# Optimization experiments

Measured on AMD Instinct MI355X. Metric: run time of the kernel, lower is better.

The kernel has to match this reference:

```python
import jax, jax.numpy as jnp
import numpy as np

B, NVEC, DIM, HEADS, DH, M, ITERS, DEPTH, NCLASS, KER = 8, 4096, 512, 8, 64, 256, 6, 2, 10, 33
INNER = HEADS * DH


def _ln(x, g, b, eps=1e-5):
    mu = x.mean(-1, keepdims=True)
    var = ((x - mu) ** 2).mean(-1, keepdims=True)
    return (x - mu) * jax.lax.rsqrt(var + eps) * g + b


def _mp_pinv(x, iters=ITERS):
    # Moore-Penrose pseudo-inverse via Newton-Schulz iterations (lucidrains).
    # x: [b, h, m, m]
    abs_x = jnp.abs(x)
    col = abs_x.sum(-1).max(-1)  # [b, h]
    row = abs_x.sum(-2).max(-1)  # [b, h]
    z = jnp.swapaxes(x, -1, -2) / (col * row)[..., None, None]
    I = jnp.eye(x.shape[-1], dtype=x.dtype)
    for _ in range(iters):
        xz = x @ z
        z = 0.25 * z @ (13.0 * I - xz @ (15.0 * I - xz @ (7.0 * I - xz)))
    return z


def _nystrom_attn(x, qkv_w, out_w, out_b, conv_w):
    b, n, _ = x.shape
    qkv = x @ qkv_w  # [b, n, 3*inner]
    q, k, v = jnp.split(qkv, 3, axis=-1)
    to_h = lambda t: t.reshape(b, n, HEADS, DH).transpose(0, 2, 1, 3)  # [b,h,n,dh]
    q, k, v = to_h(q), to_h(k), to_h(v)
    q = q * (DH ** -0.5)

    l = n // M  # tokens per landmark segment (n divisible by M)
    q_l = q.reshape(b, HEADS, M, l, DH).mean(3)  # [b,h,M,dh]
    k_l = k.reshape(b, HEADS, M, l, DH).mean(3)

    attn1 = jax.nn.softmax(jnp.einsum('bhnd,bhmd->bhnm', q, k_l), axis=-1)    # [b,h,n,M]
    attn2 = jax.nn.softmax(jnp.einsum('bhmd,bhld->bhml', q_l, k_l), axis=-1)  # [b,h,M,M]
    attn3 = jax.nn.softmax(jnp.einsum('bhmd,bhnd->bhmn', q_l, k), axis=-1)    # [b,h,M,n]

    out = (attn1 @ _mp_pinv(attn2)) @ (attn3 @ v)  # [b,h,n,dh]

    # residual depthwise conv over sequence dim (kernel 33, groups=heads, no bias)
    out = out + jax.lax.conv_general_dilated(
        v, conv_w, (1, 1), [(KER // 2, KER // 2), (0, 0)],
        dimension_numbers=('NCHW', 'OIHW', 'NCHW'), feature_group_count=HEADS)

    out = out.transpose(0, 2, 1, 3).reshape(b, n, INNER)
    return out @ out_w + out_b


def setup_inputs():
    key = jax.random.key(0)
    ks = jax.random.split(key, 12)
    s = 0.02
    f32 = jnp.float32
    return {
        'x': jax.random.normal(ks[0], (B, NVEC, 2), f32),
        'lin_w': jax.random.normal(ks[1], (2, DIM), f32) * s,
        'lin_b': jnp.zeros((DIM,), f32),
        'ln1_g': jnp.ones((DEPTH, DIM), f32),
        'ln1_b': jnp.zeros((DEPTH, DIM), f32),
        'qkv_w': jax.random.normal(ks[2], (DEPTH, DIM, 3 * INNER), f32) * s,
        'out_w': jax.random.normal(ks[3], (DEPTH, INNER, DIM), f32) * s,
        'out_b': jnp.zeros((DEPTH, DIM), f32),
        'conv_w': jax.random.normal(ks[4], (DEPTH, HEADS, 1, KER, 1), f32) * s,
        'ln2_g': jnp.ones((DEPTH, DIM), f32),
        'ln2_b': jnp.zeros((DEPTH, DIM), f32),
        'ff1_w': jax.random.normal(ks[5], (DEPTH, DIM, 4 * DIM), f32) * s,
        'ff1_b': jnp.zeros((DEPTH, 4 * DIM), f32),
        'ff2_w': jax.random.normal(ks[6], (DEPTH, 4 * DIM, DIM), f32) * s,
        'ff2_b': jnp.zeros((DEPTH, DIM), f32),
        'final_w': jax.random.normal(ks[7], (NVEC * DIM, NCLASS), f32) * s,
        'final_b': jnp.zeros((NCLASS,), f32),
    }


def reference(x, lin_w, lin_b, ln1_g, ln1_b, qkv_w, out_w, out_b, conv_w,
              ln2_g, ln2_b, ff1_w, ff1_b, ff2_w, ff2_b, final_w, final_b):
    h = x @ lin_w + lin_b  # [B, NVEC, DIM]
    for i in range(DEPTH):
        h = h + _nystrom_attn(_ln(h, ln1_g[i], ln1_b[i]), qkv_w[i], out_w[i], out_b[i], conv_w[i])
        z = _ln(h, ln2_g[i], ln2_b[i])
        h = h + (jax.nn.gelu(z @ ff1_w[i] + ff1_b[i]) @ ff2_w[i] + ff2_b[i])
    return h.reshape(h.shape[0], -1) @ final_w + final_b  # [B, NCLASS]
```

## Files before the change

kernel.cpp:

```cpp
#include <hip/hip_runtime.h>
#include <hip/hip_bf16.h>

#define BB_ 8
#define NVEC 4096
#define DIM 512
#define HEADS 8
#define DH 64
#define MM_ 256
#define ITERS 6
#define DEPTH 2
#define NCLASS 10
#define KER 33
#define INNER 512
#define LSEG 16

typedef long long ll;
typedef __bf16 bh16;
typedef __attribute__((ext_vector_type(8))) __bf16 bf16x8;
typedef __attribute__((ext_vector_type(4))) float f32x4;

template<int WR, int WC, bool TRB, bool GELU_ACT, bool RESID, bool BF16OUT,
         bool DUAL, bool SMAX, bool ADDC>
__global__ void __launch_bounds__(256)
mgemm_k(const bh16* __restrict__ A, const bh16* __restrict__ B,
        const float* __restrict__ bias, void* __restrict__ Cv, void* __restrict__ C2v,
        int K, int lda, int ldb, int ldc,
        int BI, ll sAo, ll sAi, ll sBo, ll sBi, ll sCo, ll sCi,
        int ldc2, ll sC2o, ll sC2i,
        float alpha, float diagv)
{
    constexpr int BM = WR * 64, BN = WC * 64;
    const int bz = blockIdx.z;
    const int bo = bz / BI, bi = bz % BI;
    const bh16* Ab = A + bo * sAo + (ll)bi * sAi;
    const bh16* Bb = B + bo * sBo + (ll)bi * sBi;
    const ll coff = bo * sCo + (ll)bi * sCi;

    const int gx = gridDim.x;
    const int nwg = gx * gridDim.y;
    int flat = blockIdx.y * gx + blockIdx.x;
    {
        int xcd = flat & 7, base = flat >> 3;
        int q = nwg >> 3, rr = nwg & 7;
        flat = (xcd < rr ? xcd * (q + 1) : rr * (q + 1) + (xcd - rr) * q) + base;
    }
    const int m0 = (flat / gx) * BM;
    const int n0 = (flat % gx) * BN;

    const int tid = threadIdx.x;
    const int lane = tid & 63;
    const int wave = tid >> 6;
    const int wr = wave / WC, wc = wave % WC;

    __shared__ bh16 Al[BM * 32];
    __shared__ bh16 Bl[BN * 32];
    __shared__ float srow[SMAX ? 4 * 64 : 4];

    f32x4 acc[4][4];
#pragma unroll
    for (int i = 0; i < 4; ++i)
#pragma unroll
        for (int j = 0; j < 4; ++j) acc[i][j] = (f32x4){0.f, 0.f, 0.f, 0.f};

    const int srowi = tid >> 2;
    const int ssl   = tid & 3;

    const int rsel  = ((lane & 15) >> 1) & 3;
    const int kslot = lane >> 4;

    for (int k0 = 0; k0 < K; k0 += 32) {
        __syncthreads();
#pragma unroll
        for (int i = 0; i < BM / 64; ++i) {
            int row = i * 64 + srowi;
            int gsl = ssl ^ ((row >> 1) & 3);
            __builtin_amdgcn_global_load_lds(
                (const __attribute__((address_space(1))) unsigned int*)
                    (Ab + (ll)(m0 + row) * lda + k0 + gsl * 8),
                (__attribute__((address_space(3))) unsigned int*)
                    (Al + row * 32 + ssl * 8),
                16, 0, 0);
        }
        if (!TRB) {
#pragma unroll
            for (int i = 0; i < BN / 64; ++i) {
                int row = i * 64 + srowi;
                int gsl = ssl ^ ((row >> 1) & 3);
                __builtin_amdgcn_global_load_lds(
                    (const __attribute__((address_space(1))) unsigned int*)
                        (Bb + (ll)(n0 + row) * ldb + k0 + gsl * 8),
                    (__attribute__((address_space(3))) unsigned int*)
                        (Bl + row * 32 + ssl * 8),
                    16, 0, 0);
            }
        } else {
            const int bk = tid >> 3;
            const int nb0 = (tid & 7) * (BN / 8);
#pragma unroll
            for (int v8 = 0; v8 < BN / 64; ++v8) {
                int nb = nb0 + v8 * 8;
                bf16x8 v = *(const bf16x8*)(Bb + (ll)(k0 + bk) * ldb + n0 + nb);
#pragma unroll
                for (int j = 0; j < 8; ++j) {
                    int n = nb + j;
                    int sl = (bk >> 3) ^ ((n >> 1) & 3);
                    Bl[n * 32 + sl * 8 + (bk & 7)] = v[j];
                }
            }
        }
        __syncthreads();

        bf16x8 af[4], bfr[4];
#pragma unroll
        for (int mi = 0; mi < 4; ++mi) {
            int row = wr * 64 + mi * 16 + (lane & 15);
            af[mi] = *(const bf16x8*)(Al + row * 32 + (kslot ^ rsel) * 8);
        }
#pragma unroll
        for (int ni = 0; ni < 4; ++ni) {
            int row = wc * 64 + ni * 16 + (lane & 15);
            bfr[ni] = *(const bf16x8*)(Bl + row * 32 + (kslot ^ rsel) * 8);
        }
#pragma unroll
        for (int mi = 0; mi < 4; ++mi)
#pragma unroll
            for (int ni = 0; ni < 4; ++ni)
                acc[mi][ni] = __builtin_amdgcn_mfma_f32_16x16x32_bf16(
                    af[mi], bfr[ni], acc[mi][ni], 0, 0, 0);
    }

    if (SMAX) {
        bh16* Cb = (bh16*)Cv;
#pragma unroll
        for (int mi = 0; mi < 4; ++mi)
#pragma unroll
            for (int ni = 0; ni < 4; ++ni)
#pragma unroll
                for (int r = 0; r < 4; ++r) acc[mi][ni][r] *= alpha;
        float mx[4][4];
#pragma unroll
        for (int mi = 0; mi < 4; ++mi)
#pragma unroll
            for (int r = 0; r < 4; ++r) {
                float m_ = acc[mi][0][r];
#pragma unroll
                for (int ni = 1; ni < 4; ++ni) m_ = fmaxf(m_, acc[mi][ni][r]);
#pragma unroll
                for (int msk = 1; msk < 16; msk <<= 1)
                    m_ = fmaxf(m_, __shfl_xor(m_, msk));
                mx[mi][r] = m_;
            }
        if ((lane & 15) == 0) {
#pragma unroll
            for (int mi = 0; mi < 4; ++mi)
#pragma unroll
                for (int r = 0; r < 4; ++r)
                    srow[wc * 64 + mi * 16 + (lane >> 4) * 4 + r] = mx[mi][r];
        }
        __syncthreads();
        float M_[4][4];
#pragma unroll
        for (int mi = 0; mi < 4; ++mi)
#pragma unroll
            for (int r = 0; r < 4; ++r) {
                int row = mi * 16 + (lane >> 4) * 4 + r;
                M_[mi][r] = fmaxf(fmaxf(srow[row], srow[64 + row]),
                                  fmaxf(srow[128 + row], srow[192 + row]));
            }
        __syncthreads();
        float sm[4][4];
#pragma unroll
        for (int mi = 0; mi < 4; ++mi)
#pragma unroll
            for (int r = 0; r < 4; ++r) {
                float s_ = 0.f;
#pragma unroll
                for (int ni = 0; ni < 4; ++ni) {
                    float e = __expf(acc[mi][ni][r] - M_[mi][r]);
                    acc[mi][ni][r] = e;
                    s_ += e;
                }
#pragma unroll
                for (int msk = 1; msk < 16; msk <<= 1)
                    s_ += __shfl_xor(s_, msk);
                sm[mi][r] = s_;
            }
        if ((lane & 15) == 0) {
#pragma unroll
            for (int mi = 0; mi < 4; ++mi)
#pragma unroll
                for (int r = 0; r < 4; ++r)
                    srow[wc * 64 + mi * 16 + (lane >> 4) * 4 + r] = sm[mi][r];
        }
        __syncthreads();
#pragma unroll
        for (int mi = 0; mi < 4; ++mi)
#pragma unroll
            for (int r = 0; r < 4; ++r) {
                int row = mi * 16 + (lane >> 4) * 4 + r;
                float inv = 1.0f / (srow[row] + srow[64 + row] +
                                    srow[128 + row] + srow[192 + row]);
                int rowg = m0 + row;
#pragma unroll
                for (int ni = 0; ni < 4; ++ni) {
                    int colg = n0 + wc * 64 + ni * 16 + (lane & 15);
                    Cb[coff + (ll)rowg * ldc + colg] = (bh16)(acc[mi][ni][r] * inv);
                }
            }
        return;
    }

    const ll c2off = ADDC ? (bo * sC2o + (ll)bi * sC2i) : 0;
#pragma unroll
    for (int mi = 0; mi < 4; ++mi) {
#pragma unroll
        for (int ni = 0; ni < 4; ++ni) {
            const int colg = n0 + wc * 64 + ni * 16 + (lane & 15);
            const float bia = (!DUAL && bias) ? bias[colg] : 0.f;
#pragma unroll
            for (int r = 0; r < 4; ++r) {
                const int rowg = m0 + wr * 64 + mi * 16 + (lane >> 4) * 4 + r;
                const float a = acc[mi][ni][r];
                const ll off = coff + (ll)rowg * ldc + colg;
                if (DUAL) {
                    ((bh16*)Cv)[off] = (bh16)a;
                    float w = ((rowg == colg) ? diagv : 0.f) - a;
                    ((bh16*)C2v)[off] = (bh16)w;
                } else {
                    float v = alpha * a + bia;
                    if (ADDC)
                        v += (float)((const bh16*)C2v)[c2off + (ll)rowg * ldc2 + colg];
                    if (diagv != 0.f && rowg == colg) v += diagv;
                    if (GELU_ACT) {
                        float t = tanhf(0.7978845608f * (v + 0.044715f * v * v * v));
                        v = 0.5f * v * (1.0f + t);
                    }
                    if (BF16OUT) {
                        ((bh16*)Cv)[off] = (bh16)v;
                    } else {
                        float* p = (float*)Cv + off;
                        float o = v;
                        if (RESID) o += *p;
                        *p = o;
                    }
                }
            }
        }
    }
}

template<int WR, int WC, bool TRB, bool G, bool R, bool BO, bool D, bool SX, bool AC>
static inline void mg(hipStream_t s, int M, int N, int K,
                      const bh16* A, int lda, const bh16* B, int ldb,
                      void* C, int ldc, void* C2, const float* bias,
                      int batch, int BI,
                      ll sAo, ll sAi, ll sBo, ll sBi, ll sCo, ll sCi,
                      float alpha, float diagv,
                      int ldc2 = 0, ll sC2o = 0, ll sC2i = 0)
{
    dim3 grid(N / (WC * 64), M / (WR * 64), batch);
    hipLaunchKernelGGL((mgemm_k<WR, WC, TRB, G, R, BO, D, SX, AC>), grid, dim3(256), 0, s,
                       A, B, bias, C, C2, K, lda, ldb, ldc, BI,
                       sAo, sAi, sBo, sBi, sCo, sCi, ldc2, sC2o, sC2i, alpha, diagv);
}

__global__ void embed_k(const float* __restrict__ x, const float* __restrict__ w,
                        const float* __restrict__ b, float* __restrict__ h)
{
    ll idx = (ll)blockIdx.x * 256 + threadIdx.x;
    int d = (int)(idx & 511);
    ll bn = idx >> 9;
    h[idx] = x[bn * 2] * w[d] + x[bn * 2 + 1] * w[512 + d] + b[d];
}

__global__ void __launch_bounds__(256)
ln_k(const float* __restrict__ X, const float* __restrict__ g,
     const float* __restrict__ bta, bh16* __restrict__ Y)
{
    const ll row = blockIdx.x;
    const float* x = X + row * 512;
    bh16* y = Y + row * 512;
    const int tid = threadIdx.x;
    float v0 = x[tid], v1 = x[tid + 256];
    float s = v0 + v1;
    float q = v0 * v0 + v1 * v1;
    __shared__ float sred[8];
    for (int o = 32; o; o >>= 1) { s += __shfl_down(s, o); q += __shfl_down(q, o); }
    const int lane = tid & 63, w = tid >> 6;
    if (lane == 0) { sred[w] = s; sred[4 + w] = q; }
    __syncthreads();
    float ssum = sred[0] + sred[1] + sred[2] + sred[3];
    float qsum = sred[4] + sred[5] + sred[6] + sred[7];
    float mu = ssum * (1.0f / 512.0f);
    float var = qsum * (1.0f / 512.0f) - mu * mu;
    float r = rsqrtf(var + 1e-5f);
    y[tid] = (bh16)((v0 - mu) * r * g[tid] + bta[tid]);
    y[tid + 256] = (bh16)((v1 - mu) * r * g[tid + 256] + bta[tid + 256]);
}

__global__ void __launch_bounds__(256)
cvtT_k(const float* __restrict__ in, bh16* __restrict__ outp, int C, int R)
{
    __shared__ float t[64][65];
    const int nCt = C >> 6;
    const int c0 = (blockIdx.x % nCt) * 64;
    const int r0 = (blockIdx.x / nCt) * 64;
    const int tid = threadIdx.x;
#pragma unroll
    for (int j = 0; j < 16; ++j) {
        int idx = j * 256 + tid;
        int lr = idx >> 6, lc = idx & 63;
        t[lc][lr] = in[(ll)(r0 + lr) * C + c0 + lc];
    }
    __syncthreads();
#pragma unroll
    for (int v = 0; v < 2; ++v) {
        int flat = v * 256 + tid;
        int lc = flat >> 3, r8 = (flat & 7) * 8;
        bf16x8 o;
#pragma unroll
        for (int j = 0; j < 8; ++j) o[j] = (bh16)t[lc][r8 + j];
        *(bf16x8*)(outp + (ll)(c0 + lc) * R + r0 + r8) = o;
    }
}

__global__ void landmarks_k(const bh16* __restrict__ qkv,
                            bh16* __restrict__ qlb, bh16* __restrict__ klb)
{
    int idx = blockIdx.x * 256 + threadIdx.x;
    int d = idx & 63;
    int m = (idx >> 6) & 255;
    int h = (idx >> 14) & 7;
    int b = idx >> 17;
    const bh16* base = qkv + (ll)b * (NVEC * 1536) + (ll)(m * LSEG) * 1536 + h * 64 + d;
    float sq = 0.f, sk = 0.f;
#pragma unroll
    for (int l = 0; l < LSEG; ++l) {
        sq += (float)base[(ll)l * 1536];
        sk += (float)base[(ll)l * 1536 + 512];
    }
    ll o = (ll)(b * 8 + h) * 16384 + m * 64 + d;
    qlb[o] = (bh16)(sq * (0.0625f * 0.125f));
    klb[o] = (bh16)(sk * 0.0625f);
}

__global__ void wbt_k(const bh16* __restrict__ wb, bh16* __restrict__ wbt)
{
    int idx = blockIdx.x * 256 + threadIdx.x;
    int d = idx & 63, kg = (idx >> 6) & 31, bhh = idx >> 11;
    const bh16* p = wb + (ll)bhh * 16384 + kg * 8 * 64 + d;
    bf16x8 o;
#pragma unroll
    for (int j = 0; j < 8; ++j) o[j] = p[j * 64];
    *(bf16x8*)(wbt + (ll)bhh * 16384 + d * 256 + kg * 8) = o;
}

__global__ void a3vred_k(const float* __restrict__ part, bh16* __restrict__ outp)
{
    int idx = blockIdx.x * 256 + threadIdx.x;
    int smp = idx >> 17;
    int rest = idx & 131071;
    int h = rest >> 14, o = rest & 16383;
    const float* p = part + (ll)smp * 1048576 + (ll)h * 131072 + o;
    float s = 0.f;
#pragma unroll
    for (int j = 0; j < 8; ++j) s += p[j * 16384];
    outp[(ll)(smp * 8 + h) * 16384 + o] = (bh16)s;
}

__global__ void __launch_bounds__(256)
conv_k(bh16* __restrict__ qkv, const float* __restrict__ cw)
{
    int idx = blockIdx.x * 256 + threadIdx.x;
    int c8 = idx & 63;
    int ng = (idx >> 6) & 1023;
    int b  = idx >> 16;
    const int n0 = ng * 4;
    const int h = c8 >> 3;
    const bh16* v = qkv + (ll)b * (NVEC * 1536) + 1024 + c8 * 8;

    float wreg[KER];
#pragma unroll
    for (int k = 0; k < KER; ++k) wreg[k] = cw[h * KER + k];

    float acc[4][8];
#pragma unroll
    for (int t = 0; t < 4; ++t)
#pragma unroll
        for (int e = 0; e < 8; ++e) acc[t][e] = 0.f;

#pragma unroll
    for (int m = 0; m < 36; ++m) {
        int nn = n0 + m - (KER / 2);
        bf16x8 vv = {};
        if ((unsigned)nn < (unsigned)NVEC)
            vv = *(const bf16x8*)(v + (ll)nn * 1536);
#pragma unroll
        for (int t = 0; t < 4; ++t) {
            constexpr int KMAX = KER - 1;
            int k = m - t;
            if (k >= 0 && k <= KMAX) {
                float wk = wreg[k];
#pragma unroll
                for (int e = 0; e < 8; ++e)
                    acc[t][e] = fmaf((float)vv[e], wk, acc[t][e]);
            }
        }
    }

    bh16* o = qkv + (ll)b * (NVEC * 1536) + (ll)n0 * 1536 + 512 + c8 * 8;
#pragma unroll
    for (int t = 0; t < 4; ++t) {
        bf16x8 ov;
#pragma unroll
        for (int e = 0; e < 8; ++e) ov[e] = (bh16)acc[t][e];
        *(bf16x8*)(o + (ll)t * 1536) = ov;
    }
}

__device__ __forceinline__ float blkmax(float m, float* red, int tid)
{
#pragma unroll
    for (int o = 32; o; o >>= 1) m = fmaxf(m, __shfl_down(m, o));
    if ((tid & 63) == 0) red[tid >> 6] = m;
    __syncthreads();
    m = fmaxf(fmaxf(red[0], red[1]), fmaxf(red[2], red[3]));
    __syncthreads();
    return m;
}
__device__ __forceinline__ float blksum(float s, float* red, int tid)
{
#pragma unroll
    for (int o = 32; o; o >>= 1) s += __shfl_down(s, o);
    if ((tid & 63) == 0) red[tid >> 6] = s;
    __syncthreads();
    s = red[0] + red[1] + red[2] + red[3];
    __syncthreads();
    return s;
}

__global__ void __launch_bounds__(256)
softmax_bf_k(bh16* __restrict__ X, int L)
{
    const ll row = blockIdx.x;
    bh16* x = X + row * (ll)L;
    const int tid = threadIdx.x;
    __shared__ float red[4];
    float v[16];
    bf16x8 a = *(const bf16x8*)(x + tid * 8);
    bf16x8 b = *(const bf16x8*)(x + 2048 + tid * 8);
#pragma unroll
    for (int j = 0; j < 8; ++j) { v[j] = (float)a[j]; v[8 + j] = (float)b[j]; }
    float m = -1e30f;
#pragma unroll
    for (int j = 0; j < 16; ++j) m = fmaxf(m, v[j]);
    m = blkmax(m, red, tid);
    float s = 0.f;
#pragma unroll
    for (int j = 0; j < 16; ++j) { v[j] = __expf(v[j] - m); s += v[j]; }
    s = blksum(s, red, tid);
    float inv = 1.0f / s;
    bf16x8 oa, ob;
#pragma unroll
    for (int j = 0; j < 8; ++j) { oa[j] = (bh16)(v[j] * inv); ob[j] = (bh16)(v[8 + j] * inv); }
    *(bf16x8*)(x + tid * 8) = oa;
    *(bf16x8*)(x + 2048 + tid * 8) = ob;
}

__global__ void __launch_bounds__(256)
pinv_init_k(const bh16* __restrict__ X, bh16* __restrict__ Z)
{
    const ll bh = blockIdx.x;
    const bh16* x = X + bh * 65536;
    bh16* z = Z + bh * 65536;
    const int tid = threadIdx.x;
    float rs = 0.f, cs = 0.f;
    for (int j = 0; j < 256; ++j) {
        rs += fabsf((float)x[tid * 256 + j]);
        cs += fabsf((float)x[j * 256 + tid]);
    }
    __shared__ float rbuf[256], cbuf[256];
    rbuf[tid] = rs; cbuf[tid] = cs;
    __syncthreads();
    for (int o = 128; o; o >>= 1) {
        if (tid < o) {
            rbuf[tid] = fmaxf(rbuf[tid], rbuf[tid + o]);
            cbuf[tid] = fmaxf(cbuf[tid], cbuf[tid + o]);
        }
        __syncthreads();
    }
    float inv = 1.0f / (rbuf[0] * cbuf[0]);
    for (int e = tid; e < 65536; e += 256) {
        int i = e >> 8, j = e & 255;
        z[e] = (bh16)((float)x[j * 256 + i] * inv);
    }
}

__global__ void final_init_k(const float* __restrict__ fb, float* __restrict__ out)
{
    int i = threadIdx.x;
    if (i < BB_ * NCLASS) out[i] = fb[i % NCLASS];
}

__global__ void __launch_bounds__(256)
final_gemv_k(const float* __restrict__ hbuf, const float* __restrict__ w,
             float* __restrict__ out)
{
    const int half = blockIdx.y;
    const int chunk = blockIdx.x;
    const int tid = threadIdx.x;
    const int k0 = chunk * 8192;
    float pc[4][NCLASS] = {};
    for (int e = 0; e < 32; ++e) {
        int k = k0 + e * 256 + tid;
        const float* wr = w + (ll)k * NCLASS;
        float wv[NCLASS];
#pragma unroll
        for (int c = 0; c < NCLASS; ++c) wv[c] = wr[c];
#pragma unroll
        for (int b = 0; b < 4; ++b) {
            float hv = hbuf[(ll)(half * 4 + b) * (NVEC * DIM) + k];
#pragma unroll
            for (int c = 0; c < NCLASS; ++c) pc[b][c] = fmaf(hv, wv[c], pc[b][c]);
        }
    }
    __shared__ float red[4][4][NCLASS];
    const int lane = tid & 63, wv_ = tid >> 6;
#pragma unroll
    for (int b = 0; b < 4; ++b)
#pragma unroll
        for (int c = 0; c < NCLASS; ++c) {
            float s = pc[b][c];
#pragma unroll
            for (int o = 32; o; o >>= 1) s += __shfl_down(s, o);
            if (lane == 0) red[wv_][b][c] = s;
        }
    __syncthreads();
    if (tid < 4 * NCLASS) {
        int b = tid / NCLASS, c = tid % NCLASS;
        float s = red[0][b][c] + red[1][b][c] + red[2][b][c] + red[3][b][c];
        atomicAdd(out + (half * 4 + b) * NCLASS + c, s);
    }
}

extern "C" void kernel_launch(void* const* d_in, const int* in_sizes, int n_in,
                              void* d_out, int out_size, void* d_ws, size_t ws_size,
                              hipStream_t stream)
{
    const float* x      = (const float*)d_in[0];
    const float* lin_w  = (const float*)d_in[1];
    const float* lin_b  = (const float*)d_in[2];
    const float* ln1_g  = (const float*)d_in[3];
    const float* ln1_b  = (const float*)d_in[4];
    const float* qkv_w  = (const float*)d_in[5];
    const float* out_w  = (const float*)d_in[6];
    const float* out_b  = (const float*)d_in[7];
    const float* conv_w = (const float*)d_in[8];
    const float* ln2_g  = (const float*)d_in[9];
    const float* ln2_b  = (const float*)d_in[10];
    const float* ff1_w  = (const float*)d_in[11];
    const float* ff1_b  = (const float*)d_in[12];
    const float* ff2_w  = (const float*)d_in[13];
    const float* ff2_b  = (const float*)d_in[14];
    const float* final_w = (const float*)d_in[15];
    const float* final_b = (const float*)d_in[16];
    float* out = (float*)d_out;
    float* ws  = (float*)d_ws;

    float* H    = ws;
    bh16*  QKV  = (bh16*)(ws + 16777216);
    float* P    = ws + 41943040;
    bh16*  qlbf = (bh16*)(ws + 52428800);
    bh16*  klbf = (bh16*)(ws + 52953088);
    bh16*  A3Vb = (bh16*)(ws + 53477376);
    bh16*  WBb  = (bh16*)(ws + 54001664);
    bh16*  WBT  = (bh16*)(ws + 54525952);
    bh16*  WQT  = (bh16*)(ws + 55050240);
    bh16*  WOT  = (bh16*)(ws + 55443456);
    bh16*  F1WT = (bh16*)(ws + 55574528);
    bh16*  F2WT = (bh16*)(ws + 56098816);
    if (ws_size < 56623104ULL * 4) return;

    bh16*  XLNall = (bh16*)P;
    bh16*  ATT3c  = (bh16*)P;
    float* A3Vp   = P + 8388608;
    bh16*  Xbf = (bh16*)P;
    bh16*  Z0  = (bh16*)(P + 2097152);
    bh16*  Z1  = (bh16*)(P + 4194304);
    bh16*  T1  = (bh16*)(P + 6291456);
    bh16*  T2  = (bh16*)(P + 8388608);
    bh16*  ATT1c  = (bh16*)P;
    bh16*  AOUTc  = (bh16*)(P + 8388608);
    bh16*  XLNc   = (bh16*)P;
    bh16*  HIDc   = (bh16*)(P + 2097152);

    const ll SMP = (ll)NVEC * 1536;

    hipLaunchKernelGGL(embed_k, dim3(65536), dim3(256), 0, stream, x, lin_w, lin_b, H);

    for (int i = 0; i < DEPTH; ++i) {
        const float* wq  = qkv_w + (ll)i * 512 * 1536;
        const float* wo  = out_w + (ll)i * 512 * 512;
        const float* bo  = out_b + (ll)i * 512;
        const float* cw  = conv_w + (ll)i * HEADS * KER;
        const float* g1  = ln1_g + (ll)i * 512;
        const float* b1  = ln1_b + (ll)i * 512;
        const float* g2  = ln2_g + (ll)i * 512;
        const float* b2  = ln2_b + (ll)i * 512;
        const float* f1w = ff1_w + (ll)i * 512 * 2048;
        const float* f1b = ff1_b + (ll)i * 2048;
        const float* f2w = ff2_w + (ll)i * 2048 * 512;
        const float* f2b = ff2_b + (ll)i * 512;

        hipLaunchKernelGGL(cvtT_k, dim3(192), dim3(256), 0, stream, wq, WQT, 1536, 512);
        hipLaunchKernelGGL(cvtT_k, dim3(64), dim3(256), 0, stream, wo, WOT, 512, 512);
        hipLaunchKernelGGL(cvtT_k, dim3(256), dim3(256), 0, stream, f1w, F1WT, 2048, 512);
        hipLaunchKernelGGL(cvtT_k, dim3(256), dim3(256), 0, stream, f2w, F2WT, 512, 2048);

        hipLaunchKernelGGL(ln_k, dim3(32768), dim3(256), 0, stream, H, g1, b1, XLNall);
        mg<2,2,0,0,0,1,0,0,0>(stream, 32768, 1536, 512, XLNall, 512, WQT, 512,
            QKV, 1536, nullptr, nullptr, 1, 1, 0,0, 0,0, 0,0, 1.f, 0.f);

        hipLaunchKernelGGL(landmarks_k, dim3(4096), dim3(256), 0, stream, QKV, qlbf, klbf);

        for (int c = 0; c < 4; ++c) {
            const bh16* qkvc = QKV + (ll)c * 2 * SMP;
            mg<2,2,0,0,0,1,0,0,0>(stream, 256, 4096, 64,
                qlbf + (ll)c * 262144, 64, qkvc + 512, 1536,
                ATT3c, 4096, nullptr, nullptr, 16, 8,
                131072, 16384, SMP, 64, 8388608LL, 1048576, 1.f, 0.f);
            hipLaunchKernelGGL(softmax_bf_k, dim3(4096), dim3(256), 0, stream, ATT3c, 4096);
            for (int s = 0; s < 2; ++s) {
                mg<4,1,1,0,0,0,0,0,0>(stream, 256, 64, 512,
                    ATT3c + (ll)s * 8 * 1048576, 4096, qkvc + (ll)s * SMP + 1024, 1536,
                    A3Vp + (ll)s * 1048576, 64, nullptr, nullptr, 64, 8,
                    1048576, 512, 64, 512LL * 1536, 131072, 16384, 1.f, 0.f);
            }
            hipLaunchKernelGGL(a3vred_k, dim3(1024), dim3(256), 0, stream,
                               A3Vp, A3Vb + (ll)c * 2 * 131072);
        }

        hipLaunchKernelGGL(conv_k, dim3(2048), dim3(256), 0, stream, QKV, cw);

        mg<1,4,0,0,0,1,0,1,0>(stream, 256, 256, 64, qlbf, 64, klbf, 64,
            Xbf, 256, nullptr, nullptr, 64, 64, 0, 16384, 0, 16384, 0, 65536, 1.f, 0.f);
        hipLaunchKernelGGL(pinv_init_k, dim3(64), dim3(256), 0, stream, Xbf, Z0);
        bh16* zc = Z0; bh16* zn = Z1;
        for (int it = 0; it < ITERS; ++it) {
            mg<2,2,1,0,0,1,1,0,0>(stream, 256, 256, 256, Xbf, 256, zc, 256,
                T1, 256, T2, nullptr, 64, 64, 0, 65536, 0, 65536, 0, 65536, 1.f, 7.f,
                256, 0, 65536);
            mg<2,2,1,0,0,1,0,0,0>(stream, 256, 256, 256, T1, 256, T2, 256,
                zn, 256, nullptr, nullptr, 64, 64, 0, 65536, 0, 65536, 0, 65536, -1.f, 15.f);
            mg<2,2,1,0,0,1,0,0,0>(stream, 256, 256, 256, T1, 256, zn, 256,
                T2, 256, nullptr, nullptr, 64, 64, 0, 65536, 0, 65536, 0, 65536, -1.f, 13.f);
            mg<2,2,1,0,0,1,0,0,0>(stream, 256, 256, 256, zc, 256, T2, 256,
                zn, 256, nullptr, nullptr, 64, 64, 0, 65536, 0, 65536, 0, 65536, 0.25f, 0.f);
            bh16* t = zc; zc = zn; zn = t;
        }
        mg<4,1,1,0,0,1,0,0,0>(stream, 256, 64, 256, zc, 256, A3Vb, 64,
            WBb, 64, nullptr, nullptr, 64, 64, 0, 65536, 0, 16384, 0, 16384, 1.f, 0.f);
        hipLaunchKernelGGL(wbt_k, dim3(512), dim3(256), 0, stream, WBb, WBT);

        for (int c = 0; c < 4; ++c) {
            const bh16* qkvc = QKV + (ll)c * 2 * SMP;
            mg<1,4,0,0,0,1,0,1,0>(stream, 4096, 256, 64,
                qkvc, 1536, klbf + (ll)c * 262144, 64,
                ATT1c, 256, nullptr, nullptr, 16, 8,
                SMP, 64, 131072, 16384, 8388608LL, 1048576, 0.125f, 0.f);
            mg<4,1,0,0,0,1,0,0,1>(stream, 4096, 64, 256,
                ATT1c, 256, WBT + (ll)c * 262144, 256,
                AOUTc, 512, (void*)(QKV + (ll)c * 2 * SMP + 512), nullptr, 16, 8,
                8388608LL, 1048576, 131072, 16384, 2097152LL, 64, 1.f, 0.f,
                1536, SMP, 64);
            mg<2,2,0,0,1,0,0,0,0>(stream, 8192, 512, 512, AOUTc, 512, WOT, 512,
                H + (ll)c * 2 * 2097152, 512, nullptr, bo, 1, 1, 0,0, 0,0, 0,0, 1.f, 0.f);
        }

        for (int c = 0; c < 4; ++c) {
            float* Hc = H + (ll)c * 2 * 2097152;
            hipLaunchKernelGGL(ln_k, dim3(8192), dim3(256), 0, stream, Hc, g2, b2, XLNc);
            mg<2,2,0,1,0,1,0,0,0>(stream, 8192, 2048, 512, XLNc, 512, F1WT, 512,
                HIDc, 2048, nullptr, f1b, 1, 1, 0,0, 0,0, 0,0, 1.f, 0.f);
            mg<2,2,0,0,1,0,0,0,0>(stream, 8192, 512, 2048, HIDc, 2048, F2WT, 2048,
                Hc, 512, nullptr, f2b, 1, 1, 0,0, 0,0, 0,0, 1.f, 0.f);
        }
    }

    hipLaunchKernelGGL(final_init_k, dim3(1), dim3(128), 0, stream, final_b, out);
    hipLaunchKernelGGL(final_gemv_k, dim3(256, 2), dim3(256), 0, stream, H, final_w, out);
}
```

Baseline: 3.388 ms.

## Fuse attn1 scores, softmax and WB product into one flash-style kernel

Adds a fused kernel that computes Q·K_landmark scores, the row softmax and the product with the precomputed pinv·(attn3·v) matrix in registers and LDS, then adds the conv residual and writes bf16. This removes the materialised attn1 matrix and several chunked GEMM launches, and the output projection becomes one big GEMM. The attn3 path is reorganised per batch with fp32 scores and a softmax that converts to bf16 in place, dropping the ADDC epilogue from the generic GEMM. The fused kernel uses a serialised LDS cross-wave reduction and a large shared-memory footprint, which may limit occupancy.

```diff
diff --git a/kernel.cpp b/kernel.cpp
--- a/kernel.cpp
+++ b/kernel.cpp
@@ -20,13 +20,12 @@
 typedef __attribute__((ext_vector_type(4))) float f32x4;
 
 template<int WR, int WC, bool TRB, bool GELU_ACT, bool RESID, bool BF16OUT,
-         bool DUAL, bool SMAX, bool ADDC>
+         bool DUAL, bool SMAX>
 __global__ void __launch_bounds__(256)
 mgemm_k(const bh16* __restrict__ A, const bh16* __restrict__ B,
         const float* __restrict__ bias, void* __restrict__ Cv, void* __restrict__ C2v,
         int K, int lda, int ldb, int ldc,
         int BI, ll sAo, ll sAi, ll sBo, ll sBi, ll sCo, ll sCi,
-        int ldc2, ll sC2o, ll sC2i,
         float alpha, float diagv)
 {
     constexpr int BM = WR * 64, BN = WC * 64;
@@ -210,7 +209,6 @@
         return;
     }
 
-    const ll c2off = ADDC ? (bo * sC2o + (ll)bi * sC2i) : 0;
 #pragma unroll
     for (int mi = 0; mi < 4; ++mi) {
 #pragma unroll
@@ -228,8 +226,6 @@
                     ((bh16*)C2v)[off] = (bh16)w;
                 } else {
                     float v = alpha * a + bia;
-                    if (ADDC)
-                        v += (float)((const bh16*)C2v)[c2off + (ll)rowg * ldc2 + colg];
                     if (diagv != 0.f && rowg == colg) v += diagv;
                     if (GELU_ACT) {
                         float t = tanhf(0.7978845608f * (v + 0.044715f * v * v * v));
@@ -249,19 +245,208 @@
     }
 }
 
-template<int WR, int WC, bool TRB, bool G, bool R, bool BO, bool D, bool SX, bool AC>
+template<int WR, int WC, bool TRB, bool G, bool R, bool BO, bool D, bool SX>
 static inline void mg(hipStream_t s, int M, int N, int K,
                       const bh16* A, int lda, const bh16* B, int ldb,
                       void* C, int ldc, void* C2, const float* bias,
                       int batch, int BI,
                       ll sAo, ll sAi, ll sBo, ll sBi, ll sCo, ll sCi,
-                      float alpha, float diagv,
-                      int ldc2 = 0, ll sC2o = 0, ll sC2i = 0)
+                      float alpha, float diagv)
 {
     dim3 grid(N / (WC * 64), M / (WR * 64), batch);
-    hipLaunchKernelGGL((mgemm_k<WR, WC, TRB, G, R, BO, D, SX, AC>), grid, dim3(256), 0, s,
+    hipLaunchKernelGGL((mgemm_k<WR, WC, TRB, G, R, BO, D, SX>), grid, dim3(256), 0, s,
                        A, B, bias, C, C2, K, lda, ldb, ldc, BI,
-                       sAo, sAi, sBo, sBi, sCo, sCi, ldc2, sC2o, sC2i, alpha, diagv);
+                       sAo, sAi, sBo, sBi, sCo, sCi, alpha, diagv);
+}
+
+__global__ void __launch_bounds__(256)
+fattn_k(const bh16* __restrict__ qkv, const bh16* __restrict__ klb,
+        const bh16* __restrict__ wbt, bh16* __restrict__ aout)
+{
+    const int qb = blockIdx.x;
+    const int bh = blockIdx.y;
+    const int b = bh >> 3, h = bh & 7;
+    const int q0 = qb * 64;
+    const int tid = threadIdx.x, lane = tid & 63, wave = tid >> 6;
+    const ll SMPq = (ll)NVEC * 1536;
+
+    __shared__ bh16 Pl[64 * 256];
+    __shared__ float red[64 * 64];
+    float* srow = red;
+
+    const bh16* qbase = qkv + (ll)b * SMPq + (ll)q0 * 1536 + h * 64;
+    const bh16* klbh = klb + (ll)bh * 16384;
+    const bh16* wbh  = wbt + (ll)bh * 16384;
+
+    const int kslot = lane >> 4;
+
+    f32x4 acc[4][4];
+#pragma unroll
+    for (int i = 0; i < 4; ++i)
+#pragma unroll
+        for (int j = 0; j < 4; ++j) acc[i][j] = (f32x4){0.f, 0.f, 0.f, 0.f};
+#pragma unroll
+    for (int ks = 0; ks < 2; ++ks) {
+        int k0 = ks * 32;
+        bf16x8 af[4], bfr[4];
+#pragma unroll
+        for (int mi = 0; mi < 4; ++mi) {
+            int row = mi * 16 + (lane & 15);
+            af[mi] = *(const bf16x8*)(qbase + (ll)row * 1536 + k0 + kslot * 8);
+        }
+#pragma unroll
+        for (int ni = 0; ni < 4; ++ni) {
+            int brow = wave * 64 + ni * 16 + (lane & 15);
+            bfr[ni] = *(const bf16x8*)(klbh + brow * 64 + k0 + kslot * 8);
+        }
+#pragma unroll
+        for (int mi = 0; mi < 4; ++mi)
+#pragma unroll
+            for (int ni = 0; ni < 4; ++ni)
+                acc[mi][ni] = __builtin_amdgcn_mfma_f32_16x16x32_bf16(
+                    af[mi], bfr[ni], acc[mi][ni], 0, 0, 0);
+    }
+
+#pragma unroll
+    for (int mi = 0; mi < 4; ++mi)
+#pragma unroll
+        for (int ni = 0; ni < 4; ++ni)
+#pragma unroll
+            for (int r = 0; r < 4; ++r) acc[mi][ni][r] *= 0.125f;
+    float mx[4][4];
+#pragma unroll
+    for (int mi = 0; mi < 4; ++mi)
+#pragma unroll
+        for (int r = 0; r < 4; ++r) {
+            float m_ = acc[mi][0][r];
+#pragma unroll
+            for (int ni = 1; ni < 4; ++ni) m_ = fmaxf(m_, acc[mi][ni][r]);
+#pragma unroll
+            for (int msk = 1; msk < 16; msk <<= 1)
+                m_ = fmaxf(m_, __shfl_xor(m_, msk));
+            mx[mi][r] = m_;
+        }
+    if ((lane & 15) == 0) {
+#pragma unroll
+        for (int mi = 0; mi < 4; ++mi)
+#pragma unroll
+            for (int r = 0; r < 4; ++r)
+                srow[wave * 64 + mi * 16 + (lane >> 4) * 4 + r] = mx[mi][r];
+    }
+    __syncthreads();
+    float M_[4][4];
+#pragma unroll
+    for (int mi = 0; mi < 4; ++mi)
+#pragma unroll
+        for (int r = 0; r < 4; ++r) {
+            int row = mi * 16 + (lane >> 4) * 4 + r;
+            M_[mi][r] = fmaxf(fmaxf(srow[row], srow[64 + row]),
+                              fmaxf(srow[128 + row], srow[192 + row]));
+        }
+    __syncthreads();
+    float sm[4][4];
+#pragma unroll
+    for (int mi = 0; mi < 4; ++mi)
+#pragma unroll
+        for (int r = 0; r < 4; ++r) {
+            float s_ = 0.f;
+#pragma unroll
+            for (int ni = 0; ni < 4; ++ni) {
+                float e = __expf(acc[mi][ni][r] - M_[mi][r]);
+                acc[mi][ni][r] = e;
+                s_ += e;
+            }
+#pragma unroll
+            for (int msk = 1; msk < 16; msk <<= 1)
+                s_ += __shfl_xor(s_, msk);
+            sm[mi][r] = s_;
+        }
+    if ((lane & 15) == 0) {
+#pragma unroll
+        for (int mi = 0; mi < 4; ++mi)
+#pragma unroll
+            for (int r = 0; r < 4; ++r)
+                srow[wave * 64 + mi * 16 + (lane >> 4) * 4 + r] = sm[mi][r];
+    }
+    __syncthreads();
+#pragma unroll
+    for (int mi = 0; mi < 4; ++mi)
+#pragma unroll
+        for (int r = 0; r < 4; ++r) {
+            int row = mi * 16 + (lane >> 4) * 4 + r;
+            float inv = 1.0f / (srow[row] + srow[64 + row] +
+                                srow[128 + row] + srow[192 + row]);
+            int rsw = (row >> 1) & 3;
+#pragma unroll
+            for (int ni = 0; ni < 4; ++ni) {
+                int col = wave * 64 + ni * 16 + (lane & 15);
+                int kc = col >> 5, sl = (col >> 3) & 3, e = col & 7;
+                Pl[row * 256 + kc * 32 + ((sl ^ rsw) * 8) + e] =
+                    (bh16)(acc[mi][ni][r] * inv);
+            }
+        }
+    __syncthreads();
+
+    f32x4 acc2[4][4];
+#pragma unroll
+    for (int i = 0; i < 4; ++i)
+#pragma unroll
+        for (int j = 0; j < 4; ++j) acc2[i][j] = (f32x4){0.f, 0.f, 0.f, 0.f};
+#pragma unroll
+    for (int kk = 0; kk < 2; ++kk) {
+        int k0 = wave * 64 + kk * 32;
+        int kc = k0 >> 5;
+        bf16x8 af[4], bfr[4];
+#pragma unroll
+        for (int mi = 0; mi < 4; ++mi) {
+            int row = mi * 16 + (lane & 15);
+            int rsw = (row >> 1) & 3;
+            af[mi] = *(const bf16x8*)(Pl + row * 256 + kc * 32 + ((kslot ^ rsw) * 8));
+        }
+#pragma unroll
+        for (int ni = 0; ni < 4; ++ni) {
+            int brow = ni * 16 + (lane & 15);
+            bfr[ni] = *(const bf16x8*)(wbh + brow * 256 + k0 + kslot * 8);
+        }
+#pragma unroll
+        for (int mi = 0; mi < 4; ++mi)
+#pragma unroll
+            for (int ni = 0; ni < 4; ++ni)
+                acc2[mi][ni] = __builtin_amdgcn_mfma_f32_16x16x32_bf16(
+                    af[mi], bfr[ni], acc2[mi][ni], 0, 0, 0);
+    }
+    for (int w = 0; w < 4; ++w) {
+        if (wave == w) {
+#pragma unroll
+            for (int mi = 0; mi < 4; ++mi)
+#pragma unroll
+                for (int ni = 0; ni < 4; ++ni)
+#pragma unroll
+                    for (int r = 0; r < 4; ++r) {
+                        int row = mi * 16 + (lane >> 4) * 4 + r;
+                        int col = ni * 16 + (lane & 15);
+                        if (w == 0) red[row * 64 + col] = acc2[mi][ni][r];
+                        else        red[row * 64 + col] += acc2[mi][ni][r];
+                    }
+        }
+        __syncthreads();
+    }
+    {
+        int flat = tid * 16;
+        int row = flat >> 6, col0 = flat & 63;
+        const bh16* cv = qkv + (ll)b * SMPq + (ll)(q0 + row) * 1536 + 512 + h * 64 + col0;
+        bh16* op = aout + (ll)b * (NVEC * 512) + (ll)(q0 + row) * 512 + h * 64 + col0;
+        bf16x8 c0 = *(const bf16x8*)cv;
+        bf16x8 c1 = *(const bf16x8*)(cv + 8);
+        bf16x8 o0, o1;
+#pragma unroll
+        for (int j = 0; j < 8; ++j) {
+            o0[j] = (bh16)(red[row * 64 + col0 + j] + (float)c0[j]);
+            o1[j] = (bh16)(red[row * 64 + col0 + 8 + j] + (float)c1[j]);
+        }
+        *(bf16x8*)op = o0;
+        *(bf16x8*)(op + 8) = o1;
+    }
 }
 
 __global__ void embed_k(const float* __restrict__ x, const float* __restrict__ w,
@@ -358,14 +543,12 @@
 __global__ void a3vred_k(const float* __restrict__ part, bh16* __restrict__ outp)
 {
     int idx = blockIdx.x * 256 + threadIdx.x;
-    int smp = idx >> 17;
-    int rest = idx & 131071;
-    int h = rest >> 14, o = rest & 16383;
-    const float* p = part + (ll)smp * 1048576 + (ll)h * 131072 + o;
+    int h = idx >> 14, o = idx & 16383;
+    const float* p = part + (ll)h * 131072 + o;
     float s = 0.f;
 #pragma unroll
     for (int j = 0; j < 8; ++j) s += p[j * 16384];
-    outp[(ll)(smp * 8 + h) * 16384 + o] = (bh16)s;
+    outp[idx] = (bh16)s;
 }
 
 __global__ void __launch_bounds__(256)
@@ -440,17 +623,18 @@
 }
 
 __global__ void __launch_bounds__(256)
-softmax_bf_k(bh16* __restrict__ X, int L)
+softmax_f2b_k(float* __restrict__ X)
 {
     const ll row = blockIdx.x;
-    bh16* x = X + row * (ll)L;
+    float* x = X + row * 4096;
     const int tid = threadIdx.x;
     __shared__ float red[4];
     float v[16];
-    bf16x8 a = *(const bf16x8*)(x + tid * 8);
-    bf16x8 b = *(const bf16x8*)(x + 2048 + tid * 8);
-#pragma unroll
-    for (int j = 0; j < 8; ++j) { v[j] = (float)a[j]; v[8 + j] = (float)b[j]; }
+#pragma unroll
+    for (int j = 0; j < 4; ++j) {
+        float4 t = *(const float4*)(x + tid * 16 + j * 4);
+        v[j * 4 + 0] = t.x; v[j * 4 + 1] = t.y; v[j * 4 + 2] = t.z; v[j * 4 + 3] = t.w;
+    }
     float m = -1e30f;
 #pragma unroll
     for (int j = 0; j < 16; ++j) m = fmaxf(m, v[j]);
@@ -460,11 +644,13 @@
     for (int j = 0; j < 16; ++j) { v[j] = __expf(v[j] - m); s += v[j]; }
     s = blksum(s, red, tid);
     float inv = 1.0f / s;
+    __syncthreads();
+    bh16* o = (bh16*)x;
     bf16x8 oa, ob;
 #pragma unroll
     for (int j = 0; j < 8; ++j) { oa[j] = (bh16)(v[j] * inv); ob[j] = (bh16)(v[8 + j] * inv); }
-    *(bf16x8*)(x + tid * 8) = oa;
-    *(bf16x8*)(x + 2048 + tid * 8) = ob;
+    *(bf16x8*)(o + tid * 16) = oa;
+    *(bf16x8*)(o + tid * 16 + 8) = ob;
 }
 
 __global__ void __launch_bounds__(256)
@@ -582,15 +768,14 @@
     if (ws_size < 56623104ULL * 4) return;
 
     bh16*  XLNall = (bh16*)P;
-    bh16*  ATT3c  = (bh16*)P;
+    float* SCORESf = P;
     float* A3Vp   = P + 8388608;
     bh16*  Xbf = (bh16*)P;
     bh16*  Z0  = (bh16*)(P + 2097152);
     bh16*  Z1  = (bh16*)(P + 4194304);
     bh16*  T1  = (bh16*)(P + 6291456);
     bh16*  T2  = (bh16*)(P + 8388608);
-    bh16*  ATT1c  = (bh16*)P;
-    bh16*  AOUTc  = (bh16*)(P + 8388608);
+    bh16*  AOUTa  = (bh16*)P;
     bh16*  XLNc   = (bh16*)P;
     bh16*  HIDc   = (bh16*)(P + 2097152);
 
@@ -618,71 +803,58 @@
         hipLaunchKernelGGL(cvtT_k, dim3(256), dim3(256), 0, stream, f2w, F2WT, 512, 2048);
 
         hipLaunchKernelGGL(ln_k, dim3(32768), dim3(256), 0, stream, H, g1, b1, XLNall);
-        mg<2,2,0,0,0,1,0,0,0>(stream, 32768, 1536, 512, XLNall, 512, WQT, 512,
+        mg<2,2,0,0,0,1,0,0>(stream, 32768, 1536, 512, XLNall, 512, WQT, 512,
             QKV, 1536, nullptr, nullptr, 1, 1, 0,0, 0,0, 0,0, 1.f, 0.f);
 
         hipLaunchKernelGGL(landmarks_k, dim3(4096), dim3(256), 0, stream, QKV, qlbf, klbf);
 
-        for (int c = 0; c < 4; ++c) {
-            const bh16* qkvc = QKV + (ll)c * 2 * SMP;
-            mg<2,2,0,0,0,1,0,0,0>(stream, 256, 4096, 64,
-                qlbf + (ll)c * 262144, 64, qkvc + 512, 1536,
-                ATT3c, 4096, nullptr, nullptr, 16, 8,
-                131072, 16384, SMP, 64, 8388608LL, 1048576, 1.f, 0.f);
-            hipLaunchKernelGGL(softmax_bf_k, dim3(4096), dim3(256), 0, stream, ATT3c, 4096);
-            for (int s = 0; s < 2; ++s) {
-                mg<4,1,1,0,0,0,0,0,0>(stream, 256, 64, 512,
-                    ATT3c + (ll)s * 8 * 1048576, 4096, qkvc + (ll)s * SMP + 1024, 1536,
-                    A3Vp + (ll)s * 1048576, 64, nullptr, nullptr, 64, 8,
-                    1048576, 512, 64, 512LL * 1536, 131072, 16384, 1.f, 0.f);
-            }
-            hipLaunchKernelGGL(a3vred_k, dim3(1024), dim3(256), 0, stream,
-                               A3Vp, A3Vb + (ll)c * 2 * 131072);
+        for (int b = 0; b < BB_; ++b) {
+            const bh16* qkvb = QKV + (ll)b * SMP;
+            mg<2,2,0,0,0,0,0,0>(stream, 256, 4096, 64,
+                qlbf + (ll)b * 131072, 64, qkvb + 512, 1536,
+                SCORESf, 4096, nullptr, nullptr, 8, 8,
+                0, 16384, 0, 64, 0, 1048576, 1.f, 0.f);
+            hipLaunchKernelGGL(softmax_f2b_k, dim3(2048), dim3(256), 0, stream, SCORESf);
+            mg<4,1,1,0,0,0,0,0>(stream, 256, 64, 512,
+                (const bh16*)SCORESf, 8192, qkvb + 1024, 1536,
+                A3Vp, 64, nullptr, nullptr, 64, 8,
+                2097152, 512, 64, 512LL * 1536, 131072, 16384, 1.f, 0.f);
+            hipLaunchKernelGGL(a3vred_k, dim3(512), dim3(256), 0, stream,
+                               A3Vp, A3Vb + (ll)b * 131072);
         }
 
         hipLaunchKernelGGL(conv_k, dim3(2048), dim3(256), 0, stream, QKV, cw);
 
-        mg<1,4,0,0,0,1,0,1,0>(stream, 256, 256, 64, qlbf, 64, klbf, 64,
+        mg<1,4,0,0,0,1,0,1>(stream, 256, 256, 64, qlbf, 64, klbf, 64,
             Xbf, 256, nullptr, nullptr, 64, 64, 0, 16384, 0, 16384, 0, 65536, 1.f, 0.f);
         hipLaunchKernelGGL(pinv_init_k, dim3(64), dim3(256), 0, stream, Xbf, Z0);
         bh16* zc = Z0; bh16* zn = Z1;
         for (int it = 0; it < ITERS; ++it) {
-            mg<2,2,1,0,0,1,1,0,0>(stream, 256, 256, 256, Xbf, 256, zc, 256,
-                T1, 256, T2, nullptr, 64, 64, 0, 65536, 0, 65536, 0, 65536, 1.f, 7.f,
-                256, 0, 65536);
-            mg<2,2,1,0,0,1,0,0,0>(stream, 256, 256, 256, T1, 256, T2, 256,
+            mg<2,2,1,0,0,1,1,0>(stream, 256, 256, 256, Xbf, 256, zc, 256,
+                T1, 256, T2, nullptr, 64, 64, 0, 65536, 0, 65536, 0, 65536, 1.f, 7.f);
+            mg<2,2,1,0,0,1,0,0>(stream, 256, 256, 256, T1, 256, T2, 256,
                 zn, 256, nullptr, nullptr, 64, 64, 0, 65536, 0, 65536, 0, 65536, -1.f, 15.f);
-            mg<2,2,1,0,0,1,0,0,0>(stream, 256, 256, 256, T1, 256, zn, 256,
+            mg<2,2,1,0,0,1,0,0>(stream, 256, 256, 256, T1, 256, zn, 256,
                 T2, 256, nullptr, nullptr, 64, 64, 0, 65536, 0, 65536, 0, 65536, -1.f, 13.f);
-            mg<2,2,1,0,0,1,0,0,0>(stream, 256, 256, 256, zc, 256, T2, 256,
+            mg<2,2,1,0,0,1,0,0>(stream, 256, 256, 256, zc, 256, T2, 256,
                 zn, 256, nullptr, nullptr, 64, 64, 0, 65536, 0, 65536, 0, 65536, 0.25f, 0.f);
             bh16* t = zc; zc = zn; zn = t;
         }
-        mg<4,1,1,0,0,1,0,0,0>(stream, 256, 64, 256, zc, 256, A3Vb, 64,
+        mg<4,1,1,0,0,1,0,0>(stream, 256, 64, 256, zc, 256, A3Vb, 64,
             WBb, 64, nullptr, nullptr, 64, 64, 0, 65536, 0, 16384, 0, 16384, 1.f, 0.f);
         hipLaunchKernelGGL(wbt_k, dim3(512), dim3(256), 0, stream, WBb, WBT);
 
-        for (int c = 0; c < 4; ++c) {
-            const bh16* qkvc = QKV + (ll)c * 2 * SMP;
-            mg<1,4,0,0,0,1,0,1,0>(stream, 4096, 256, 64,
-                qkvc, 1536, klbf + (ll)c * 262144, 64,
-                ATT1c, 256, nullptr, nullptr, 16, 8,
-                SMP, 64, 131072, 16384, 8388608LL, 1048576, 0.125f, 0.f);
-            mg<4,1,0,0,0,1,0,0,1>(stream, 4096, 64, 256,
-                ATT1c, 256, WBT + (ll)c * 262144, 256,
-                AOUTc, 512, (void*)(QKV + (ll)c * 2 * SMP + 512), nullptr, 16, 8,
-                8388608LL, 1048576, 131072, 16384, 2097152LL, 64, 1.f, 0.f,
-                1536, SMP, 64);
-            mg<2,2,0,0,1,0,0,0,0>(stream, 8192, 512, 512, AOUTc, 512, WOT, 512,
-                H + (ll)c * 2 * 2097152, 512, nullptr, bo, 1, 1, 0,0, 0,0, 0,0, 1.f, 0.f);
-        }
+        hipLaunchKernelGGL(fattn_k, dim3(64, 64), dim3(256), 0, stream,
+                           QKV, klbf, WBT, AOUTa);
+        mg<2,2,0,0,1,0,0,0>(stream, 32768, 512, 512, AOUTa, 512, WOT, 512,
+            H, 512, nullptr, bo, 1, 1, 0,0, 0,0, 0,0, 1.f, 0.f);
 
         for (int c = 0; c < 4; ++c) {
             float* Hc = H + (ll)c * 2 * 2097152;
             hipLaunchKernelGGL(ln_k, dim3(8192), dim3(256), 0, stream, Hc, g2, b2, XLNc);
-            mg<2,2,0,1,0,1,0,0,0>(stream, 8192, 2048, 512, XLNc, 512, F1WT, 512,
+            mg<2,2,0,1,0,1,0,0>(stream, 8192, 2048, 512, XLNc, 512, F1WT, 512,
                 HIDc, 2048, nullptr, f1b, 1, 1, 0,0, 0,0, 0,0, 1.f, 0.f);
-            mg<2,2,0,0,1,0,0,0,0>(stream, 8192, 512, 2048, HIDc, 2048, F2WT, 2048,
+            mg<2,2,0,0,1,0,0,0>(stream, 8192, 512, 2048, HIDc, 2048, F2WT, 2048,
                 Hc, 512, nullptr, f2b, 1, 1, 0,0, 0,0, 0,0, 1.f, 0.f);
         }
     }
```

After: 3.317 ms. 2.1% less time.
